# Kernel tuning notes

Hardware: AMD Instinct MI355X
Metric: run time of the kernel (lower is better)

The kernel has to match this reference:

```python
import jax, jax.numpy as jnp
import numpy as np

N_NODES = 100000
N_EDGES = 1600000
NEG_SLOPE = 0.2


def _gat_conv(x, src, dst, W, att_src, att_dst, bias, heads, ch, concat):
    # x: [N, F_in]; W: [F_in, heads*ch]; att_*: [heads, ch]; bias: [heads*ch] or [ch]
    h = (x @ W).reshape(-1, heads, ch)                       # [N, H, C]
    a_src = jnp.einsum('nhc,hc->nh', h, att_src)             # [N, H]
    a_dst = jnp.einsum('nhc,hc->nh', h, att_dst)             # [N, H]
    e = jax.nn.leaky_relu(a_src[src] + a_dst[dst], NEG_SLOPE)  # [E, H]
    # segment softmax over incoming edges of each destination node
    m = jax.ops.segment_max(e, dst, num_segments=N_NODES)     # [N, H]
    ex = jnp.exp(e - m[dst])
    den = jax.ops.segment_sum(ex, dst, num_segments=N_NODES)
    alpha = ex / (den[dst] + 1e-16)                            # [E, H]
    out = jax.ops.segment_sum(alpha[:, :, None] * h[src], dst, num_segments=N_NODES)  # [N, H, C]
    out = out.reshape(-1, heads * ch) if concat else out.mean(axis=1)
    return out + bias


def setup_inputs() -> dict:
    key = jax.random.key(0)
    ks = jax.random.split(key, 20)

    def glorot(k, shape):
        fan = sum(shape[-2:]) if len(shape) > 1 else shape[-1]
        return jax.random.normal(k, shape, jnp.float32) * jnp.sqrt(2.0 / fan)

    x = jax.random.normal(ks[0], (N_NODES, 14), jnp.float32)
    edge_index = jax.random.randint(ks[1], (2, N_EDGES), 0, N_NODES, dtype=jnp.int32)

    return {
        'x': x,
        'edge_index': edge_index,
        # conv1: 14 -> 32, 4 heads, concat
        'W1': glorot(ks[2], (14, 128)), 'as1': glorot(ks[3], (4, 32)), 'ad1': glorot(ks[4], (4, 32)),
        'b1': jnp.zeros((128,), jnp.float32),
        # conv2: 128 -> 32, 4 heads, concat
        'W2': glorot(ks[5], (128, 128)), 'as2': glorot(ks[6], (4, 32)), 'ad2': glorot(ks[7], (4, 32)),
        'b2': jnp.zeros((128,), jnp.float32),
        # conv3: 128 -> 32, 1 head, no concat
        'W3': glorot(ks[8], (128, 32)), 'as3': glorot(ks[9], (1, 32)), 'ad3': glorot(ks[10], (1, 32)),
        'b3': jnp.zeros((32,), jnp.float32),
        # head Linear(32, 1)
        'head_w': glorot(ks[11], (32, 1)),
        'head_b': jnp.zeros((1,), jnp.float32),
    }


def reference(x, edge_index, W1, as1, ad1, b1, W2, as2, ad2, b2, W3, as3, ad3, b3, head_w, head_b):
    # add self loops once (PyG add_self_loops=True, same edge set each layer)
    loops = jnp.arange(N_NODES, dtype=edge_index.dtype)
    src = jnp.concatenate([edge_index[0], loops])
    dst = jnp.concatenate([edge_index[1], loops])

    h = jax.nn.elu(_gat_conv(x, src, dst, W1, as1, ad1, b1, heads=4, ch=32, concat=True))
    # dropout p=0.3 is identity in eval mode
    h = jax.nn.elu(_gat_conv(h, src, dst, W2, as2, ad2, b2, heads=4, ch=32, concat=True))
    h = jax.nn.elu(_gat_conv(h, src, dst, W3, as3, ad3, b3, heads=1, ch=32, concat=False))
    return (h @ head_w + head_b).squeeze(-1)  # [N]
```

## Files before the change

### kernel.cpp

```cpp
#include <hip/hip_runtime.h>
#include <hip/hip_fp16.h>

#define NEG_SLOPE 0.2f
#define CH4 128
#define CH3 128
#define BKCAP 2688
#define EPB 32

typedef _Float16 f16;
typedef _Float16 f16x4 __attribute__((ext_vector_type(4)));
typedef _Float16 f16x8 __attribute__((ext_vector_type(8)));
typedef float f32x4 __attribute__((ext_vector_type(4)));

__device__ __forceinline__ float elu1f(float x) { return x > 0.f ? x : __expf(x) - 1.f; }

__global__ __launch_bounds__(256) void part1(const int* __restrict__ src,
                                             const int* __restrict__ dst, int E,
                                             int* __restrict__ bcur, int* __restrict__ stg) {
    __shared__ int hist[1024];
    __shared__ int base[1024];
    int t = threadIdx.x;
    for (int i = t; i < 1024; i += 256) hist[i] = 0;
    __syncthreads();
    int e0 = blockIdx.x * (256 * EPB);
    int ed[EPB];
    int br[EPB];
#pragma unroll
    for (int j = 0; j < EPB; ++j) {
        int e = e0 + t + j * 256;
        if (e < E) {
            int s = src[e], d = dst[e];
            ed[j] = (s << 7) | (d & 127);
            int b = d >> 7;
            br[j] = (b << 13) | atomicAdd(&hist[b], 1);
        } else br[j] = -1;
    }
    __syncthreads();
    for (int i = t; i < 1024; i += 256) {
        int h = hist[i];
        base[i] = h ? atomicAdd(&bcur[i], h) : 0;
    }
    __syncthreads();
#pragma unroll
    for (int j = 0; j < EPB; ++j) {
        if (br[j] >= 0) {
            int b = br[j] >> 13, r = br[j] & 0x1FFF;
            stg[(size_t)b * BKCAP + base[b] + r] = ed[j];
        }
    }
}

__global__ __launch_bounds__(256) void bucket_scan(const int* __restrict__ bcur,
                                                   int* __restrict__ bbase,
                                                   int* __restrict__ rpN,
                                                   int N, int NBK, int Etot) {
    __shared__ int sd[256];
    int t = threadIdx.x;
    int loc[4]; int s = 0;
#pragma unroll
    for (int j = 0; j < 4; ++j) {
        int b = t * 4 + j;
        int v = 0;
        if (b < NBK) {
            int nodes = N - (b << 7);
            nodes = nodes > 128 ? 128 : nodes;
            v = bcur[b] + nodes;
        }
        loc[j] = v; s += v;
    }
    sd[t] = s; __syncthreads();
    for (int o = 1; o < 256; o <<= 1) {
        int x = (t >= o) ? sd[t - o] : 0;
        __syncthreads();
        sd[t] += x;
        __syncthreads();
    }
    int pre = sd[t] - s;
#pragma unroll
    for (int j = 0; j < 4; ++j) {
        int b = t * 4 + j;
        if (b < NBK) { bbase[b] = pre; pre += loc[j]; }
    }
    if (t == 0) *rpN = Etot;
}

__global__ __launch_bounds__(256) void part2f(const int* __restrict__ stg,
                                              const int* __restrict__ bcur,
                                              const int* __restrict__ bbase,
                                              int* __restrict__ rp,
                                              int* __restrict__ csr_src, int N) {
    __shared__ int h[128];
    __shared__ int pref[128];
    int b = blockIdx.x, t = threadIdx.x;
    int node0 = b << 7;
    if (t < 128) h[t] = 1;
    __syncthreads();
    int c = bcur[b];
    const int* sb = stg + (size_t)b * BKCAP;
    for (int i = t; i < c; i += 256) atomicAdd(&h[sb[i] & 127], 1);
    __syncthreads();
    if (t < 128) pref[t] = h[t];
    __syncthreads();
    for (int o = 1; o < 128; o <<= 1) {
        int v = 0;
        if (t < 128 && t >= o) v = pref[t - o];
        __syncthreads();
        if (t < 128) pref[t] += v;
        __syncthreads();
    }
    int base = bbase[b];
    if (t < 128) {
        int node = node0 + t;
        if (node < N) {
            int r = base + pref[t] - h[t];
            rp[node] = r;
            csr_src[r] = node;
            h[t] = r + 1;
        }
    }
    __syncthreads();
    for (int i = t; i < c; i += 256) {
        int p = sb[i];
        int pos = atomicAdd(&h[p & 127], 1);
        csr_src[pos] = p >> 7;
    }
}

__global__ void prep_k(int* __restrict__ bcur, const float* __restrict__ W2,
                       const float* __restrict__ W3, f16* __restrict__ W2t,
                       f16* __restrict__ W3t) {
    int i = blockIdx.x * 256 + threadIdx.x;
    if (i < 1024) bcur[i] = 0;
    if (i < 16384) { int k = i >> 7, c = i & 127; W2t[c * 128 + k] = (f16)W2[i]; }
    if (i < 4096)  { int k = i >> 5, c = i & 31;  W3t[c * 128 + k] = (f16)W3[i]; }
}

__global__ void node1_k(const float* __restrict__ x, const float* __restrict__ W1,
                        const float* __restrict__ as1, const float* __restrict__ ad1,
                        f16* __restrict__ Hh, float* __restrict__ a_s,
                        float* __restrict__ a_d, int N) {
    const int NB = 8;
    __shared__ float sx[NB][14];
    int nb = blockIdx.x * NB;
    int tid = threadIdx.x;
    if (tid < NB * 14) {
        int j = tid / 14, f = tid % 14;
        int n = nb + j;
        sx[j][f] = (n < N) ? x[n * 14 + f] : 0.f;
    }
    __syncthreads();
    float satt = as1[tid], datt = ad1[tid];
    for (int j = 0; j < NB; ++j) {
        int n = nb + j;
        if (n >= N) break;
        float acc = 0.f;
#pragma unroll
        for (int f = 0; f < 14; ++f) acc += sx[j][f] * W1[f * 128 + tid];
        Hh[(size_t)n * 128 + tid] = (f16)acc;
        float vs = acc * satt, vd = acc * datt;
#pragma unroll
        for (int o = 16; o > 0; o >>= 1) {
            vs += __shfl_xor(vs, o, 32);
            vd += __shfl_xor(vd, o, 32);
        }
        if ((tid & 31) == 0) {
            int h = tid >> 5;
            a_s[n * 4 + h] = vs;
            a_d[n * 4 + h] = vd;
        }
    }
}

__global__ __launch_bounds__(256) void node2_mfma(
        const f16* __restrict__ A, const f16* __restrict__ Bt,
        const float* __restrict__ as_, const float* __restrict__ ad_,
        f16* __restrict__ Hh, float* __restrict__ a_s, float* __restrict__ a_d, int N) {
    __shared__ f16 Ah[64 * 128];
    __shared__ f16 Bh[128 * 128];
    int t = threadIdx.x;
    int row0 = blockIdx.x * 64;
#pragma unroll
    for (int i = 0; i < 4; ++i) {
        int gi = t + 256 * i;
        int r = gi >> 4, g = gi & 15;
        int gr = row0 + r;
        f16x8 v = {};
        if (gr < N) v = *(const f16x8*)(A + (size_t)gr * 128 + g * 8);
        *(f16x8*)&Ah[r * 128 + ((g ^ (r & 7)) << 3)] = v;
    }
#pragma unroll
    for (int i = 0; i < 8; ++i) {
        int gi = t + 256 * i;
        int c = gi >> 4, g = gi & 15;
        f16x8 v = *(const f16x8*)(Bt + c * 128 + g * 8);
        *(f16x8*)&Bh[c * 128 + ((g ^ (c & 7)) << 3)] = v;
    }
    __syncthreads();

    int wv = t >> 6, l = t & 63;
    int lrow = wv * 16 + (l & 15);
    int kq = l >> 4;
    f32x4 acc[8];
#pragma unroll
    for (int nf = 0; nf < 8; ++nf) acc[nf] = (f32x4){0.f, 0.f, 0.f, 0.f};
#pragma unroll
    for (int kk = 0; kk < 4; ++kk) {
        int gk = kk * 4 + kq;
        f16x8 a = *(f16x8*)&Ah[lrow * 128 + ((gk ^ (lrow & 7)) << 3)];
#pragma unroll
        for (int nf = 0; nf < 8; ++nf) {
            int col = nf * 16 + (l & 15);
            f16x8 b = *(f16x8*)&Bh[col * 128 + ((gk ^ (col & 7)) << 3)];
            acc[nf] = __builtin_amdgcn_mfma_f32_16x16x32_f16(a, b, acc[nf], 0, 0, 0);
        }
    }
    int colb = l & 15, rq = l >> 4;
#pragma unroll
    for (int j = 0; j < 4; ++j) {
        int row = row0 + wv * 16 + rq * 4 + j;
        bool ok = row < N;
        if (ok) {
#pragma unroll
            for (int nf = 0; nf < 8; ++nf)
                Hh[(size_t)row * 128 + nf * 16 + colb] = (f16)acc[nf][j];
        }
#pragma unroll
        for (int h = 0; h < 4; ++h) {
            float vs = acc[2 * h][j] * as_[h * 32 + colb] + acc[2 * h + 1][j] * as_[h * 32 + 16 + colb];
            float vd = acc[2 * h][j] * ad_[h * 32 + colb] + acc[2 * h + 1][j] * ad_[h * 32 + 16 + colb];
#pragma unroll
            for (int o = 8; o > 0; o >>= 1) {
                vs += __shfl_xor(vs, o);
                vd += __shfl_xor(vd, o);
            }
            if (ok && colb == 0) {
                a_s[row * 4 + h] = vs;
                a_d[row * 4 + h] = vd;
            }
        }
    }
}

__global__ __launch_bounds__(256) void node3_mfma(
        const f16* __restrict__ A, const f16* __restrict__ Bt,
        const float* __restrict__ as3, const float* __restrict__ ad3,
        f16* __restrict__ H3h, float* __restrict__ a_s, float* __restrict__ a_d, int N) {
    __shared__ f16 Ah[64 * 128];
    __shared__ f16 Bh[32 * 128];
    int t = threadIdx.x;
    int row0 = blockIdx.x * 64;
#pragma unroll
    for (int i = 0; i < 4; ++i) {
        int gi = t + 256 * i;
        int r = gi >> 4, g = gi & 15;
        int gr = row0 + r;
        f16x8 v = {};
        if (gr < N) v = *(const f16x8*)(A + (size_t)gr * 128 + g * 8);
        *(f16x8*)&Ah[r * 128 + ((g ^ (r & 7)) << 3)] = v;
    }
#pragma unroll
    for (int i = 0; i < 2; ++i) {
        int gi = t + 256 * i;
        int c = gi >> 4, g = gi & 15;
        f16x8 v = *(const f16x8*)(Bt + c * 128 + g * 8);
        *(f16x8*)&Bh[c * 128 + ((g ^ (c & 7)) << 3)] = v;
    }
    __syncthreads();

    int wv = t >> 6, l = t & 63;
    int lrow = wv * 16 + (l & 15);
    int kq = l >> 4;
    f32x4 acc[2];
    acc[0] = (f32x4){0.f, 0.f, 0.f, 0.f};
    acc[1] = (f32x4){0.f, 0.f, 0.f, 0.f};
#pragma unroll
    for (int kk = 0; kk < 4; ++kk) {
        int gk = kk * 4 + kq;
        f16x8 a = *(f16x8*)&Ah[lrow * 128 + ((gk ^ (lrow & 7)) << 3)];
#pragma unroll
        for (int nf = 0; nf < 2; ++nf) {
            int col = nf * 16 + (l & 15);
            f16x8 b = *(f16x8*)&Bh[col * 128 + ((gk ^ (col & 7)) << 3)];
            acc[nf] = __builtin_amdgcn_mfma_f32_16x16x32_f16(a, b, acc[nf], 0, 0, 0);
        }
    }
    int colb = l & 15, rq = l >> 4;
#pragma unroll
    for (int j = 0; j < 4; ++j) {
        int row = row0 + wv * 16 + rq * 4 + j;
        bool ok = row < N;
        if (ok) {
            H3h[(size_t)row * 32 + colb] = (f16)acc[0][j];
            H3h[(size_t)row * 32 + 16 + colb] = (f16)acc[1][j];
        }
        float vs = acc[0][j] * as3[colb] + acc[1][j] * as3[16 + colb];
        float vd = acc[0][j] * ad3[colb] + acc[1][j] * ad3[16 + colb];
#pragma unroll
        for (int o = 8; o > 0; o >>= 1) {
            vs += __shfl_xor(vs, o);
            vd += __shfl_xor(vd, o);
        }
        if (ok && colb == 0) { a_s[row] = vs; a_d[row] = vd; }
    }
}

__global__ __launch_bounds__(256) void gat_edge4(
        const int* __restrict__ rp, const int* __restrict__ cs,
        const float* __restrict__ a_s, const float* __restrict__ a_d,
        const f16* __restrict__ Hh, const float* __restrict__ bias,
        f16* __restrict__ O2, int N) {
    __shared__ int   s_lds[4][CH4 + 8];
    __shared__ float w_lds[4][CH4 + 8][4];
    __shared__ float rd_lds[4][4];
    int t = threadIdx.x;
    int wv = t >> 6, l = t & 63;
    int hg = l >> 4, l16 = l & 15;
    int n = blockIdx.x * 4 + wv;
    if (n >= N) return;
    int beg = rp[n];
    int deg = min(rp[n + 1] - beg, CH4);
    float a_dh = a_d[n * 4 + hg];

    float ss = 0.f;
    for (int i = l16; i < deg; i += 16) {
        int s = cs[beg + i];
        if (hg == 0) s_lds[wv][i] = s << 8;
        float e0 = a_s[s * 4 + hg] + a_dh;
        float e = fminf(fmaxf(e0, NEG_SLOPE * e0), 80.f);
        float w = __expf(e);
        w_lds[wv][i][hg] = w;
        ss += w;
    }
    if (l < 8) {
        int ip = deg + l;
        s_lds[wv][ip] = 0;
        w_lds[wv][ip][0] = 0.f;
        w_lds[wv][ip][1] = 0.f;
        w_lds[wv][ip][2] = 0.f;
        w_lds[wv][ip][3] = 0.f;
    }
#pragma unroll
    for (int o = 8; o > 0; o >>= 1) ss += __shfl_xor(ss, o);
    if (l16 == 0) rd_lds[wv][hg] = 1.f / (ss + 1e-16f);

    __builtin_amdgcn_sched_barrier(0);

    int g = l >> 4, li = l & 15;
    int hd = li >> 2;
    int choff = li * 16;
    float ac0 = 0.f, ac1 = 0.f, ac2 = 0.f, ac3 = 0.f;
    float ac4 = 0.f, ac5 = 0.f, ac6 = 0.f, ac7 = 0.f;
    int D8 = (deg + 7) & ~7;
    for (int i = 0; i < D8; i += 8) {
        int sb0 = s_lds[wv][i + g];
        int sb1 = s_lds[wv][i + 4 + g];
        float w0 = w_lds[wv][i + g][hd];
        float w1 = w_lds[wv][i + 4 + g][hd];
        f16x8 v0 = *(const f16x8*)((const char*)Hh + (size_t)(unsigned)(sb0 + choff));
        f16x8 v1 = *(const f16x8*)((const char*)Hh + (size_t)(unsigned)(sb1 + choff));
        ac0 += w0 * (float)v0[0]; ac1 += w0 * (float)v0[1];
        ac2 += w0 * (float)v0[2]; ac3 += w0 * (float)v0[3];
        ac4 += w0 * (float)v0[4]; ac5 += w0 * (float)v0[5];
        ac6 += w0 * (float)v0[6]; ac7 += w0 * (float)v0[7];
        ac0 += w1 * (float)v1[0]; ac1 += w1 * (float)v1[1];
        ac2 += w1 * (float)v1[2]; ac3 += w1 * (float)v1[3];
        ac4 += w1 * (float)v1[4]; ac5 += w1 * (float)v1[5];
        ac6 += w1 * (float)v1[6]; ac7 += w1 * (float)v1[7];
    }
    ac0 += __shfl_xor(ac0, 16); ac0 += __shfl_xor(ac0, 32);
    ac1 += __shfl_xor(ac1, 16); ac1 += __shfl_xor(ac1, 32);
    ac2 += __shfl_xor(ac2, 16); ac2 += __shfl_xor(ac2, 32);
    ac3 += __shfl_xor(ac3, 16); ac3 += __shfl_xor(ac3, 32);
    ac4 += __shfl_xor(ac4, 16); ac4 += __shfl_xor(ac4, 32);
    ac5 += __shfl_xor(ac5, 16); ac5 += __shfl_xor(ac5, 32);
    ac6 += __shfl_xor(ac6, 16); ac6 += __shfl_xor(ac6, 32);
    ac7 += __shfl_xor(ac7, 16); ac7 += __shfl_xor(ac7, 32);

    if (g == 0) {
        float rdv = rd_lds[wv][hd];
        const float4* b4 = (const float4*)bias;
        float4 bb0 = b4[li * 2], bb1 = b4[li * 2 + 1];
        f16x8 ov;
        ov[0] = (f16)elu1f(ac0 * rdv + bb0.x);
        ov[1] = (f16)elu1f(ac1 * rdv + bb0.y);
        ov[2] = (f16)elu1f(ac2 * rdv + bb0.z);
        ov[3] = (f16)elu1f(ac3 * rdv + bb0.w);
        ov[4] = (f16)elu1f(ac4 * rdv + bb1.x);
        ov[5] = (f16)elu1f(ac5 * rdv + bb1.y);
        ov[6] = (f16)elu1f(ac6 * rdv + bb1.z);
        ov[7] = (f16)elu1f(ac7 * rdv + bb1.w);
        *(f16x8*)(O2 + (size_t)n * 128 + li * 8) = ov;
    }
}

__global__ __launch_bounds__(256) void gat_edge3(
        const int* __restrict__ rp, const int* __restrict__ cs,
        const float* __restrict__ a_s, const float* __restrict__ a_d,
        const f16* __restrict__ H3, const float* __restrict__ b3,
        const float* __restrict__ hw, const float* __restrict__ hb,
        float* __restrict__ out, int N) {
    __shared__ int   s_lds[16][CH3 + 8];
    __shared__ float w_lds[16][CH3 + 8];
    __shared__ float rd_lds[16];
    int t = threadIdx.x;
    int wv = t >> 6, l = t & 63;
    int nl = l >> 4, l16 = l & 15;
    int slot = wv * 4 + nl;
    int n = blockIdx.x * 16 + slot;
    if (n >= N) return;
    int beg = rp[n];
    int deg = min(rp[n + 1] - beg, CH3);
    float a_dh = a_d[n];

    float ss = 0.f;
    for (int i = l16; i < deg; i += 16) {
        int s = cs[beg + i];
        s_lds[slot][i] = s << 6;
        float e0 = a_s[s] + a_dh;
        float e = fminf(fmaxf(e0, NEG_SLOPE * e0), 80.f);
        float w = __expf(e);
        w_lds[slot][i] = w;
        ss += w;
    }
    if (l16 < 4) {
        int ip = deg + l16;
        s_lds[slot][ip] = 0;
        w_lds[slot][ip] = 0.f;
    }
    ss += __shfl_xor(ss, 8);
    ss += __shfl_xor(ss, 4);
    ss += __shfl_xor(ss, 2);
    ss += __shfl_xor(ss, 1);
    if (l16 == 0) rd_lds[slot] = 1.f / (ss + 1e-16f);

    __builtin_amdgcn_sched_barrier(0);

    int g2 = l16 >> 3, li = l16 & 7;
    int choff = li * 8;
    float ac0 = 0.f, ac1 = 0.f, ac2 = 0.f, ac3 = 0.f;
    int D4 = (deg + 3) & ~3;
    int sb0 = s_lds[slot][g2], sb1 = s_lds[slot][2 + g2];
    float w0 = w_lds[slot][g2], w1 = w_lds[slot][2 + g2];
    f16x4 v0 = *(const f16x4*)((const char*)H3 + (size_t)(unsigned)(sb0 + choff));
    f16x4 v1 = *(const f16x4*)((const char*)H3 + (size_t)(unsigned)(sb1 + choff));
    int i = 0;
    for (; i + 4 < D4; i += 4) {
        int nb0 = s_lds[slot][i + 4 + g2];
        int nb1 = s_lds[slot][i + 6 + g2];
        float nw0 = w_lds[slot][i + 4 + g2];
        float nw1 = w_lds[slot][i + 6 + g2];
        f16x4 n0 = *(const f16x4*)((const char*)H3 + (size_t)(unsigned)(nb0 + choff));
        f16x4 n1 = *(const f16x4*)((const char*)H3 + (size_t)(unsigned)(nb1 + choff));
        ac0 += w0 * (float)v0[0]; ac1 += w0 * (float)v0[1];
        ac2 += w0 * (float)v0[2]; ac3 += w0 * (float)v0[3];
        ac0 += w1 * (float)v1[0]; ac1 += w1 * (float)v1[1];
        ac2 += w1 * (float)v1[2]; ac3 += w1 * (float)v1[3];
        v0 = n0; v1 = n1; w0 = nw0; w1 = nw1;
    }
    ac0 += w0 * (float)v0[0]; ac1 += w0 * (float)v0[1];
    ac2 += w0 * (float)v0[2]; ac3 += w0 * (float)v0[3];
    ac0 += w1 * (float)v1[0]; ac1 += w1 * (float)v1[1];
    ac2 += w1 * (float)v1[2]; ac3 += w1 * (float)v1[3];
    ac0 += __shfl_xor(ac0, 8);
    ac1 += __shfl_xor(ac1, 8);
    ac2 += __shfl_xor(ac2, 8);
    ac3 += __shfl_xor(ac3, 8);

    if (g2 == 0) {
        float rdv = rd_lds[slot];
        int c = li * 4;
        float v = elu1f(ac0 * rdv + b3[c])     * hw[c]
                + elu1f(ac1 * rdv + b3[c + 1]) * hw[c + 1]
                + elu1f(ac2 * rdv + b3[c + 2]) * hw[c + 2]
                + elu1f(ac3 * rdv + b3[c + 3]) * hw[c + 3];
        v += __shfl_xor(v, 4);
        v += __shfl_xor(v, 2);
        v += __shfl_xor(v, 1);
        if (l16 == 0) out[n] = v + hb[0];
    }
}

extern "C" void kernel_launch(void* const* d_in, const int* in_sizes, int n_in,
                              void* d_out, int out_size, void* d_ws, size_t ws_size,
                              hipStream_t stream) {
    const float* x   = (const float*)d_in[0];
    const int*   ei  = (const int*)d_in[1];
    const float* W1  = (const float*)d_in[2];
    const float* as1 = (const float*)d_in[3];
    const float* ad1 = (const float*)d_in[4];
    const float* b1  = (const float*)d_in[5];
    const float* W2  = (const float*)d_in[6];
    const float* as2 = (const float*)d_in[7];
    const float* ad2 = (const float*)d_in[8];
    const float* b2  = (const float*)d_in[9];
    const float* W3  = (const float*)d_in[10];
    const float* as3 = (const float*)d_in[11];
    const float* ad3 = (const float*)d_in[12];
    const float* b3  = (const float*)d_in[13];
    const float* hw  = (const float*)d_in[14];
    const float* hb  = (const float*)d_in[15];

    const int N = in_sizes[0] / 14;
    const int E = in_sizes[1] / 2;
    const int Etot = E + N;
    const int* src = ei;
    const int* dst = ei + E;
    const int NBK = (N + 127) >> 7;

    float* ws  = (float*)d_ws;
    f16* Hh  = (f16*)ws;
    f16* O2  = (f16*)(ws + (size_t)N * 64);
    float* a_s = ws + (size_t)N * 128;
    float* a_d = a_s + (size_t)N * 4;
    f16* W2t = (f16*)(a_d + (size_t)N * 4);
    f16* W3t = W2t + 16384;
    int* stg = (int*)(W3t + 4096);
    int* bcur    = stg + (size_t)NBK * BKCAP;
    int* bbase   = bcur + 1024;
    int* rp      = bbase + 1024;
    int* csr_src = rp + (N + 1);

    dim3 blk128(128), blk256(256);
    const int GB = (N + 63) / 64;
    const int P1B = (E + 256 * EPB - 1) / (256 * EPB);

    prep_k<<<64, blk256, 0, stream>>>(bcur, W2, W3, W2t, W3t);
    part1<<<P1B, blk256, 0, stream>>>(src, dst, E, bcur, stg);
    bucket_scan<<<1, blk256, 0, stream>>>(bcur, bbase, rp + N, N, NBK, Etot);
    part2f<<<NBK, blk256, 0, stream>>>(stg, bcur, bbase, rp, csr_src, N);

    node1_k<<<(N + 7) / 8, blk128, 0, stream>>>(x, W1, as1, ad1, Hh, a_s, a_d, N);
    gat_edge4<<<(N + 3) / 4, blk256, 0, stream>>>(rp, csr_src, a_s, a_d, Hh, b1, O2, N);

    node2_mfma<<<GB, blk256, 0, stream>>>(O2, W2t, as2, ad2, Hh, a_s, a_d, N);
    gat_edge4<<<(N + 3) / 4, blk256, 0, stream>>>(rp, csr_src, a_s, a_d, Hh, b2, O2, N);

    node3_mfma<<<GB, blk256, 0, stream>>>(O2, W3t, as3, ad3, Hh, a_s, a_d, N);
    gat_edge3<<<(N + 15) / 16, blk256, 0, stream>>>(rp, csr_src, a_s, a_d,
                                                    Hh, b3, hw, hb,
                                                    (float*)d_out, N);
}
```

Measured before the change: 296.2 us.

## Fold attention vectors into GEMM weights and pack edge src/weight into int2 LDS

Precomputes W·att_src and W·att_dst as extra output columns of the layer-2 and layer-3 weight matrices, so the MFMA GEMM produces the attention logits directly. This removes the per-row shuffle reductions and attention-vector loads in the GEMM epilogue. The edge kernels also store source offset and weight together as one int2 in LDS, so each neighbour needs a single LDS read instead of two. In exchange each GEMM does one extra MFMA column tile, and the logits now come from fp16-rounded folded weights, which slightly changes precision.

Result: faster. 285.7 us (-3.5%).

```diff
diff --git a/kernel.cpp b/kernel.cpp
--- a/kernel.cpp
+++ b/kernel.cpp
@@ -126,13 +126,46 @@
     }
 }
 
-__global__ void prep_k(int* __restrict__ bcur, const float* __restrict__ W2,
-                       const float* __restrict__ W3, f16* __restrict__ W2t,
-                       f16* __restrict__ W3t) {
+__global__ void prep_k(int* __restrict__ bcur,
+                       const float* __restrict__ W2, const float* __restrict__ W3,
+                       const float* __restrict__ as2, const float* __restrict__ ad2,
+                       const float* __restrict__ as3, const float* __restrict__ ad3,
+                       f16* __restrict__ W2te, f16* __restrict__ W3te) {
     int i = blockIdx.x * 256 + threadIdx.x;
     if (i < 1024) bcur[i] = 0;
-    if (i < 16384) { int k = i >> 7, c = i & 127; W2t[c * 128 + k] = (f16)W2[i]; }
-    if (i < 4096)  { int k = i >> 5, c = i & 31;  W3t[c * 128 + k] = (f16)W3[i]; }
+    if (i < 16384) { int k = i >> 7, c = i & 127; W2te[c * 128 + k] = (f16)W2[i]; }
+    if (i < 1024) {
+        int col = i >> 7, k = i & 127;
+        const float* att = (col < 4) ? as2 : ad2;
+        int h = col & 3;
+        float acc = 0.f;
+#pragma unroll
+        for (int c = 0; c < 32; ++c) acc += W2[k * 128 + h * 32 + c] * att[h * 32 + c];
+        W2te[(128 + col) * 128 + k] = (f16)acc;
+    }
+    if (i >= 1024 && i < 2048) {
+        int j = i - 1024;
+        W2te[(136 + (j >> 7)) * 128 + (j & 127)] = (f16)0.f;
+    }
+    if (i < 4096) { int k = i >> 5, c = i & 31; W3te[c * 128 + k] = (f16)W3[i]; }
+    if (i >= 4096 && i < 4224) {
+        int k = i - 4096;
+        float acc = 0.f;
+#pragma unroll
+        for (int c = 0; c < 32; ++c) acc += W3[k * 32 + c] * as3[c];
+        W3te[32 * 128 + k] = (f16)acc;
+    }
+    if (i >= 4224 && i < 4352) {
+        int k = i - 4224;
+        float acc = 0.f;
+#pragma unroll
+        for (int c = 0; c < 32; ++c) acc += W3[k * 32 + c] * ad3[c];
+        W3te[33 * 128 + k] = (f16)acc;
+    }
+    if (i >= 4352 && i < 6144) {
+        int j = i - 4352;
+        W3te[(34 + (j >> 7)) * 128 + (j & 127)] = (f16)0.f;
+    }
 }
 
 __global__ void node1_k(const float* __restrict__ x, const float* __restrict__ W1,
@@ -173,10 +206,9 @@
 
 __global__ __launch_bounds__(256) void node2_mfma(
         const f16* __restrict__ A, const f16* __restrict__ Bt,
-        const float* __restrict__ as_, const float* __restrict__ ad_,
         f16* __restrict__ Hh, float* __restrict__ a_s, float* __restrict__ a_d, int N) {
     __shared__ f16 Ah[64 * 128];
-    __shared__ f16 Bh[128 * 128];
+    __shared__ f16 Bh[144 * 128];
     int t = threadIdx.x;
     int row0 = blockIdx.x * 64;
 #pragma unroll
@@ -189,7 +221,7 @@
         *(f16x8*)&Ah[r * 128 + ((g ^ (r & 7)) << 3)] = v;
     }
 #pragma unroll
-    for (int i = 0; i < 8; ++i) {
+    for (int i = 0; i < 9; ++i) {
         int gi = t + 256 * i;
         int c = gi >> 4, g = gi & 15;
         f16x8 v = *(const f16x8*)(Bt + c * 128 + g * 8);
@@ -200,15 +232,15 @@
     int wv = t >> 6, l = t & 63;
     int lrow = wv * 16 + (l & 15);
     int kq = l >> 4;
-    f32x4 acc[8];
-#pragma unroll
-    for (int nf = 0; nf < 8; ++nf) acc[nf] = (f32x4){0.f, 0.f, 0.f, 0.f};
+    f32x4 acc[9];
+#pragma unroll
+    for (int nf = 0; nf < 9; ++nf) acc[nf] = (f32x4){0.f, 0.f, 0.f, 0.f};
 #pragma unroll
     for (int kk = 0; kk < 4; ++kk) {
         int gk = kk * 4 + kq;
         f16x8 a = *(f16x8*)&Ah[lrow * 128 + ((gk ^ (lrow & 7)) << 3)];
 #pragma unroll
-        for (int nf = 0; nf < 8; ++nf) {
+        for (int nf = 0; nf < 9; ++nf) {
             int col = nf * 16 + (l & 15);
             f16x8 b = *(f16x8*)&Bh[col * 128 + ((gk ^ (col & 7)) << 3)];
             acc[nf] = __builtin_amdgcn_mfma_f32_16x16x32_f16(a, b, acc[nf], 0, 0, 0);
@@ -218,35 +250,20 @@
 #pragma unroll
     for (int j = 0; j < 4; ++j) {
         int row = row0 + wv * 16 + rq * 4 + j;
-        bool ok = row < N;
-        if (ok) {
-#pragma unroll
-            for (int nf = 0; nf < 8; ++nf)
-                Hh[(size_t)row * 128 + nf * 16 + colb] = (f16)acc[nf][j];
-        }
-#pragma unroll
-        for (int h = 0; h < 4; ++h) {
-            float vs = acc[2 * h][j] * as_[h * 32 + colb] + acc[2 * h + 1][j] * as_[h * 32 + 16 + colb];
-            float vd = acc[2 * h][j] * ad_[h * 32 + colb] + acc[2 * h + 1][j] * ad_[h * 32 + 16 + colb];
-#pragma unroll
-            for (int o = 8; o > 0; o >>= 1) {
-                vs += __shfl_xor(vs, o);
-                vd += __shfl_xor(vd, o);
-            }
-            if (ok && colb == 0) {
-                a_s[row * 4 + h] = vs;
-                a_d[row * 4 + h] = vd;
-            }
-        }
+        if (row >= N) continue;
+#pragma unroll
+        for (int nf = 0; nf < 8; ++nf)
+            Hh[(size_t)row * 128 + nf * 16 + colb] = (f16)acc[nf][j];
+        if (colb < 4)      a_s[row * 4 + colb] = acc[8][j];
+        else if (colb < 8) a_d[row * 4 + colb - 4] = acc[8][j];
     }
 }
 
 __global__ __launch_bounds__(256) void node3_mfma(
         const f16* __restrict__ A, const f16* __restrict__ Bt,
-        const float* __restrict__ as3, const float* __restrict__ ad3,
         f16* __restrict__ H3h, float* __restrict__ a_s, float* __restrict__ a_d, int N) {
     __shared__ f16 Ah[64 * 128];
-    __shared__ f16 Bh[32 * 128];
+    __shared__ f16 Bh[48 * 128];
     int t = threadIdx.x;
     int row0 = blockIdx.x * 64;
 #pragma unroll
@@ -259,7 +276,7 @@
         *(f16x8*)&Ah[r * 128 + ((g ^ (r & 7)) << 3)] = v;
     }
 #pragma unroll
-    for (int i = 0; i < 2; ++i) {
+    for (int i = 0; i < 3; ++i) {
         int gi = t + 256 * i;
         int c = gi >> 4, g = gi & 15;
         f16x8 v = *(const f16x8*)(Bt + c * 128 + g * 8);
@@ -270,15 +287,15 @@
     int wv = t >> 6, l = t & 63;
     int lrow = wv * 16 + (l & 15);
     int kq = l >> 4;
-    f32x4 acc[2];
-    acc[0] = (f32x4){0.f, 0.f, 0.f, 0.f};
-    acc[1] = (f32x4){0.f, 0.f, 0.f, 0.f};
+    f32x4 acc[3];
+#pragma unroll
+    for (int nf = 0; nf < 3; ++nf) acc[nf] = (f32x4){0.f, 0.f, 0.f, 0.f};
 #pragma unroll
     for (int kk = 0; kk < 4; ++kk) {
         int gk = kk * 4 + kq;
         f16x8 a = *(f16x8*)&Ah[lrow * 128 + ((gk ^ (lrow & 7)) << 3)];
 #pragma unroll
-        for (int nf = 0; nf < 2; ++nf) {
+        for (int nf = 0; nf < 3; ++nf) {
             int col = nf * 16 + (l & 15);
             f16x8 b = *(f16x8*)&Bh[col * 128 + ((gk ^ (col & 7)) << 3)];
             acc[nf] = __builtin_amdgcn_mfma_f32_16x16x32_f16(a, b, acc[nf], 0, 0, 0);
@@ -288,19 +305,11 @@
 #pragma unroll
     for (int j = 0; j < 4; ++j) {
         int row = row0 + wv * 16 + rq * 4 + j;
-        bool ok = row < N;
-        if (ok) {
-            H3h[(size_t)row * 32 + colb] = (f16)acc[0][j];
-            H3h[(size_t)row * 32 + 16 + colb] = (f16)acc[1][j];
-        }
-        float vs = acc[0][j] * as3[colb] + acc[1][j] * as3[16 + colb];
-        float vd = acc[0][j] * ad3[colb] + acc[1][j] * ad3[16 + colb];
-#pragma unroll
-        for (int o = 8; o > 0; o >>= 1) {
-            vs += __shfl_xor(vs, o);
-            vd += __shfl_xor(vd, o);
-        }
-        if (ok && colb == 0) { a_s[row] = vs; a_d[row] = vd; }
+        if (row >= N) continue;
+        H3h[(size_t)row * 32 + colb] = (f16)acc[0][j];
+        H3h[(size_t)row * 32 + 16 + colb] = (f16)acc[1][j];
+        if (colb == 0) a_s[row] = acc[2][j];
+        else if (colb == 1) a_d[row] = acc[2][j];
     }
 }
 
@@ -309,8 +318,7 @@
         const float* __restrict__ a_s, const float* __restrict__ a_d,
         const f16* __restrict__ Hh, const float* __restrict__ bias,
         f16* __restrict__ O2, int N) {
-    __shared__ int   s_lds[4][CH4 + 8];
-    __shared__ float w_lds[4][CH4 + 8][4];
+    __shared__ int2  sw_lds[4][CH4 + 8][4];
     __shared__ float rd_lds[4][4];
     int t = threadIdx.x;
     int wv = t >> 6, l = t & 63;
@@ -324,20 +332,18 @@
     float ss = 0.f;
     for (int i = l16; i < deg; i += 16) {
         int s = cs[beg + i];
-        if (hg == 0) s_lds[wv][i] = s << 8;
         float e0 = a_s[s * 4 + hg] + a_dh;
         float e = fminf(fmaxf(e0, NEG_SLOPE * e0), 80.f);
         float w = __expf(e);
-        w_lds[wv][i][hg] = w;
+        sw_lds[wv][i][hg] = make_int2(s << 8, __float_as_int(w));
         ss += w;
     }
     if (l < 8) {
         int ip = deg + l;
-        s_lds[wv][ip] = 0;
-        w_lds[wv][ip][0] = 0.f;
-        w_lds[wv][ip][1] = 0.f;
-        w_lds[wv][ip][2] = 0.f;
-        w_lds[wv][ip][3] = 0.f;
+        sw_lds[wv][ip][0] = make_int2(0, 0);
+        sw_lds[wv][ip][1] = make_int2(0, 0);
+        sw_lds[wv][ip][2] = make_int2(0, 0);
+        sw_lds[wv][ip][3] = make_int2(0, 0);
     }
 #pragma unroll
     for (int o = 8; o > 0; o >>= 1) ss += __shfl_xor(ss, o);
@@ -352,12 +358,12 @@
     float ac4 = 0.f, ac5 = 0.f, ac6 = 0.f, ac7 = 0.f;
     int D8 = (deg + 7) & ~7;
     for (int i = 0; i < D8; i += 8) {
-        int sb0 = s_lds[wv][i + g];
-        int sb1 = s_lds[wv][i + 4 + g];
-        float w0 = w_lds[wv][i + g][hd];
-        float w1 = w_lds[wv][i + 4 + g][hd];
-        f16x8 v0 = *(const f16x8*)((const char*)Hh + (size_t)(unsigned)(sb0 + choff));
-        f16x8 v1 = *(const f16x8*)((const char*)Hh + (size_t)(unsigned)(sb1 + choff));
+        int2 p0 = sw_lds[wv][i + g][hd];
+        int2 p1 = sw_lds[wv][i + 4 + g][hd];
+        float w0 = __int_as_float(p0.y);
+        float w1 = __int_as_float(p1.y);
+        f16x8 v0 = *(const f16x8*)((const char*)Hh + (size_t)(unsigned)(p0.x + choff));
+        f16x8 v1 = *(const f16x8*)((const char*)Hh + (size_t)(unsigned)(p1.x + choff));
         ac0 += w0 * (float)v0[0]; ac1 += w0 * (float)v0[1];
         ac2 += w0 * (float)v0[2]; ac3 += w0 * (float)v0[3];
         ac4 += w0 * (float)v0[4]; ac5 += w0 * (float)v0[5];
@@ -399,8 +405,7 @@
         const f16* __restrict__ H3, const float* __restrict__ b3,
         const float* __restrict__ hw, const float* __restrict__ hb,
         float* __restrict__ out, int N) {
-    __shared__ int   s_lds[16][CH3 + 8];
-    __shared__ float w_lds[16][CH3 + 8];
+    __shared__ int2  sw_lds[16][CH3 + 8];
     __shared__ float rd_lds[16];
     int t = threadIdx.x;
     int wv = t >> 6, l = t & 63;
@@ -415,17 +420,15 @@
     float ss = 0.f;
     for (int i = l16; i < deg; i += 16) {
         int s = cs[beg + i];
-        s_lds[slot][i] = s << 6;
         float e0 = a_s[s] + a_dh;
         float e = fminf(fmaxf(e0, NEG_SLOPE * e0), 80.f);
         float w = __expf(e);
-        w_lds[slot][i] = w;
+        sw_lds[slot][i] = make_int2(s << 6, __float_as_int(w));
         ss += w;
     }
     if (l16 < 4) {
         int ip = deg + l16;
-        s_lds[slot][ip] = 0;
-        w_lds[slot][ip] = 0.f;
+        sw_lds[slot][ip] = make_int2(0, 0);
     }
     ss += __shfl_xor(ss, 8);
     ss += __shfl_xor(ss, 4);
@@ -439,18 +442,17 @@
     int choff = li * 8;
     float ac0 = 0.f, ac1 = 0.f, ac2 = 0.f, ac3 = 0.f;
     int D4 = (deg + 3) & ~3;
-    int sb0 = s_lds[slot][g2], sb1 = s_lds[slot][2 + g2];
-    float w0 = w_lds[slot][g2], w1 = w_lds[slot][2 + g2];
-    f16x4 v0 = *(const f16x4*)((const char*)H3 + (size_t)(unsigned)(sb0 + choff));
-    f16x4 v1 = *(const f16x4*)((const char*)H3 + (size_t)(unsigned)(sb1 + choff));
+    int2 p0 = sw_lds[slot][g2], p1 = sw_lds[slot][2 + g2];
+    float w0 = __int_as_float(p0.y), w1 = __int_as_float(p1.y);
+    f16x4 v0 = *(const f16x4*)((const char*)H3 + (size_t)(unsigned)(p0.x + choff));
+    f16x4 v1 = *(const f16x4*)((const char*)H3 + (size_t)(unsigned)(p1.x + choff));
     int i = 0;
     for (; i + 4 < D4; i += 4) {
-        int nb0 = s_lds[slot][i + 4 + g2];
-        int nb1 = s_lds[slot][i + 6 + g2];
-        float nw0 = w_lds[slot][i + 4 + g2];
-        float nw1 = w_lds[slot][i + 6 + g2];
-        f16x4 n0 = *(const f16x4*)((const char*)H3 + (size_t)(unsigned)(nb0 + choff));
-        f16x4 n1 = *(const f16x4*)((const char*)H3 + (size_t)(unsigned)(nb1 + choff));
+        int2 q0 = sw_lds[slot][i + 4 + g2];
+        int2 q1 = sw_lds[slot][i + 6 + g2];
+        float nw0 = __int_as_float(q0.y), nw1 = __int_as_float(q1.y);
+        f16x4 n0 = *(const f16x4*)((const char*)H3 + (size_t)(unsigned)(q0.x + choff));
+        f16x4 n1 = *(const f16x4*)((const char*)H3 + (size_t)(unsigned)(q1.x + choff));
         ac0 += w0 * (float)v0[0]; ac1 += w0 * (float)v0[1];
         ac2 += w0 * (float)v0[2]; ac3 += w0 * (float)v0[3];
         ac0 += w1 * (float)v1[0]; ac1 += w1 * (float)v1[1];
@@ -512,9 +514,9 @@
     f16* O2  = (f16*)(ws + (size_t)N * 64);
     float* a_s = ws + (size_t)N * 128;
     float* a_d = a_s + (size_t)N * 4;
-    f16* W2t = (f16*)(a_d + (size_t)N * 4);
-    f16* W3t = W2t + 16384;
-    int* stg = (int*)(W3t + 4096);
+    f16* W2te = (f16*)(a_d + (size_t)N * 4);
+    f16* W3te = W2te + 18432;
+    int* stg = (int*)(W3te + 6144);
     int* bcur    = stg + (size_t)NBK * BKCAP;
     int* bbase   = bcur + 1024;
     int* rp      = bbase + 1024;
@@ -524,7 +526,7 @@
     const int GB = (N + 63) / 64;
     const int P1B = (E + 256 * EPB - 1) / (256 * EPB);
 
-    prep_k<<<64, blk256, 0, stream>>>(bcur, W2, W3, W2t, W3t);
+    prep_k<<<64, blk256, 0, stream>>>(bcur, W2, W3, as2, ad2, as3, ad3, W2te, W3te);
     part1<<<P1B, blk256, 0, stream>>>(src, dst, E, bcur, stg);
     bucket_scan<<<1, blk256, 0, stream>>>(bcur, bbase, rp + N, N, NBK, Etot);
     part2f<<<NBK, blk256, 0, stream>>>(stg, bcur, bbase, rp, csr_src, N);
@@ -532,10 +534,10 @@
     node1_k<<<(N + 7) / 8, blk128, 0, stream>>>(x, W1, as1, ad1, Hh, a_s, a_d, N);
     gat_edge4<<<(N + 3) / 4, blk256, 0, stream>>>(rp, csr_src, a_s, a_d, Hh, b1, O2, N);
 
-    node2_mfma<<<GB, blk256, 0, stream>>>(O2, W2t, as2, ad2, Hh, a_s, a_d, N);
+    node2_mfma<<<GB, blk256, 0, stream>>>(O2, W2te, Hh, a_s, a_d, N);
     gat_edge4<<<(N + 3) / 4, blk256, 0, stream>>>(rp, csr_src, a_s, a_d, Hh, b2, O2, N);
 
-    node3_mfma<<<GB, blk256, 0, stream>>>(O2, W3t, as3, ad3, Hh, a_s, a_d, N);
+    node3_mfma<<<GB, blk256, 0, stream>>>(O2, W3te, Hh, a_s, a_d, N);
     gat_edge3<<<(N + 15) / 16, blk256, 0, stream>>>(rp, csr_src, a_s, a_d,
                                                     Hh, b3, hw, hb,
                                                     (float*)d_out, N);
```
